# Optimization experiments

Measured on AMD Instinct MI355X. Metric: run time of the kernel, lower is better.

Reference implementation:

```python
import jax, jax.numpy as jnp
import numpy as np
from jax import lax

B, C, H, W = 32, 64, 56, 56
G = 4            # num_heads*2 with num_heads=2
SMK, K = 5, 7
C2 = C // 2
HEAD_DIM = C // G
SCALE = HEAD_DIM ** -0.5


def _bias_idx(k, h, w):
    # static replica of ContMix.generate_idx + apply_rpb index construction
    rpb_size = 2 * k - 1
    idx_h = np.arange(k)
    idx_w = np.arange(k)
    idx_k = (idx_h[:, None] * rpb_size + idx_w).reshape(-1)
    rep_h = np.ones(k, np.int64); rep_h[k // 2] = h - (k - 1)
    rep_w = np.ones(k, np.int64); rep_w[k // 2] = w - (k - 1)
    bias_hw = np.repeat(idx_h, rep_h)[:, None] * rpb_size + np.repeat(idx_w, rep_w)  # (h, w)
    bias_idx = (bias_hw[..., None] + idx_k).reshape(-1, k * k)[::-1]  # torch.flip dim 0
    return jnp.asarray(bias_idx.copy())

IDX1 = _bias_idx(SMK, H, W)
IDX2 = _bias_idx(K, H, W)


def setup_inputs() -> dict:
    key = jax.random.key(0)
    ks = jax.random.split(key, 18)
    r = lambda i, sh: jax.random.normal(ks[i], sh, jnp.float32)
    return dict(
        x=r(0, (B, C, H, W)),
        lepe_w=r(1, (C, 1, K, K)) * 0.1,
        lepe_b=r(2, (C,)) * 0.1,
        lepe_bn_s=1.0 + 0.1 * r(3, (C,)),
        lepe_bn_b=0.1 * r(4, (C,)),
        wq_w=r(5, (C2, C2)) * (C2 ** -0.5),
        wq_bn_s=1.0 + 0.1 * r(6, (C2,)),
        wq_bn_b=0.1 * r(7, (C2,)),
        wk_w=r(8, (C2, C2)) * (C2 ** -0.5),
        wk_bn_s=1.0 + 0.1 * r(9, (C2,)),
        wk_bn_b=0.1 * r(10, (C2,)),
        wp_w=r(11, (SMK * SMK + K * K, 49)) * (49 ** -0.5),
        wp_b=0.1 * r(12, (SMK * SMK + K * K,)),
        rpb1=0.02 * r(13, (G, 2 * SMK - 1, 2 * SMK - 1)),
        rpb2=0.02 * r(14, (G, 2 * K - 1, 2 * K - 1)),
        dy_w=r(15, (C, C)) * (C ** -0.5),
        dy_bn_s=1.0 + 0.1 * r(16, (C,)),
        dy_bn_b=0.1 * r(17, (C,)),
    )


def _per_ch(t):
    return t[None, :, None, None]


def _contmix(x, lepe_w, lepe_b, lepe_bn_s, lepe_bn_b, wq_w, wq_bn_s, wq_bn_b,
             wk_w, wk_bn_s, wk_bn_b, wp_w, wp_b, rpb1, rpb2, dy_w, dy_bn_s, dy_bn_b):
    # lepe: deploy-mode DilatedReparamBlock = depthwise 7x7 conv (+bias), then eval BN
    lepe = lax.conv_general_dilated(x, lepe_w, (1, 1), [(K // 2, K // 2)] * 2,
                                    feature_group_count=C)
    lepe = (lepe + _per_ch(lepe_b)) * _per_ch(lepe_bn_s) + _per_ch(lepe_bn_b)

    q, kf = jnp.split(x, 2, axis=1)                         # (B, C2, H, W) each
    q = jnp.einsum('oi,bihw->bohw', wq_w, q)                # weight_query 1x1 conv
    q = (q * _per_ch(wq_bn_s) + _per_ch(wq_bn_b)) * SCALE
    # weight_key: AdaptiveAvgPool2d(7) -> 1x1 conv -> BN (H,W divisible by 7)
    kp = kf.reshape(B, C2, 7, H // 7, 7, W // 7).mean(axis=(3, 5))
    kp = jnp.einsum('oi,bihw->bohw', wk_w, kp)
    kp = kp * _per_ch(wk_bn_s) + _per_ch(wk_bn_b)

    qg = q.reshape(B, G, C2 // G, H * W)                    # b g c n
    kg = kp.reshape(B, G, C2 // G, 49)                      # b g c l
    w = jnp.einsum('bgcn,bgcl->bgnl', qg, kg)               # (B, G, HW, 49)
    # weight_proj: 1x1 conv over the 49 pooled-context channels
    w = jnp.einsum('ml,bgnl->bgnm', wp_w, w) + wp_b         # (B, G, HW, 74)
    w = w.reshape(B, G, H, W, SMK * SMK + K * K)

    attn1 = w[..., :SMK * SMK]
    attn2 = w[..., SMK * SMK:]
    attn1 = attn1 + rpb1.reshape(G, -1)[:, IDX1].reshape(1, G, H, W, SMK * SMK)
    attn2 = attn2 + rpb2.reshape(G, -1)[:, IDX2].reshape(1, G, H, W, K * K)
    attn1 = jax.nn.softmax(attn1, axis=-1)
    attn2 = jax.nn.softmax(attn2, axis=-1)

    c = C // (2 * G)                                        # value head dim = 8
    v = x.reshape(B, 2, G, c, H, W)                         # 'b (m g c) h w'

    def dyn_mix(attn, val, k):
        # unfold + einsum: content-adaptive depthwise mixing
        p = lax.conv_general_dilated_patches(
            val.reshape(B, G * c, H, W), (k, k), (1, 1), [(k // 2, k // 2)] * 2,
            dimension_numbers=('NCHW', 'OIHW', 'NCHW'))
        p = p.reshape(B, G, c, k * k, H, W)                 # channel-major patch layout
        return jnp.einsum('bgckhw,bghwk->bgchw', p, attn)

    x1 = dyn_mix(attn1, v[:, 0], SMK)
    x2 = dyn_mix(attn2, v[:, 1], K)
    out = jnp.concatenate([x1, x2], axis=1).reshape(B, C, H, W)
    out = jnp.einsum('oi,bihw->bohw', dy_w, out)            # dyconv_proj 1x1 + BN
    out = out * _per_ch(dy_bn_s) + _per_ch(dy_bn_b)
    return out + lepe


def reference(x, lepe_w, lepe_b, lepe_bn_s, lepe_bn_b, wq_w, wq_bn_s, wq_bn_b,
              wk_w, wk_bn_s, wk_bn_b, wp_w, wp_b, rpb1, rpb2, dy_w, dy_bn_s, dy_bn_b):
    return _contmix(x, lepe_w, lepe_b, lepe_bn_s, lepe_bn_b, wq_w, wq_bn_s, wq_bn_b,
                    wk_w, wk_bn_s, wk_bn_b, wp_w, wp_b, rpb1, rpb2, dy_w, dy_bn_s, dy_bn_b)
```

## Files before the change

kernel.cpp:

```cpp
#include <hip/hip_runtime.h>

#define BB 32
#define CC 64
#define HH 56
#define WW 56
#define HW 3136
#define TW 64
#define TR 12

__global__ __launch_bounds__(256) void prep_k(const float* __restrict__ x,
                                              const float* __restrict__ wk,
                                              const float* __restrict__ wks,
                                              const float* __restrict__ wkb,
                                              const float* __restrict__ wp_w,
                                              float* __restrict__ WK) {
    __shared__ float p_s[32 * 49];
    __shared__ float kg_s[8 * 49];
    const int b = blockIdx.x >> 2;
    const int g = blockIdx.x & 3;
    const int tid = threadIdx.x;
    for (int idx = tid; idx < 1568; idx += 256) {
        const int i = idx / 49, l = idx % 49;
        const int py = l / 7, px = l % 7;
        const float4* xp4 = reinterpret_cast<const float4*>(
            x + ((long)(b * CC + 32 + i)) * HW + py * 8 * WW + px * 8);
        float4 sA = make_float4(0.f, 0.f, 0.f, 0.f);
        float4 sB = make_float4(0.f, 0.f, 0.f, 0.f);
        #pragma unroll
        for (int y = 0; y < 8; ++y) {
            const float4 a = xp4[y * 14];
            const float4 c = xp4[y * 14 + 1];
            sA.x += a.x; sA.y += a.y; sA.z += a.z; sA.w += a.w;
            sB.x += c.x; sB.y += c.y; sB.z += c.z; sB.w += c.w;
        }
        p_s[idx] = (sA.x + sA.y + sA.z + sA.w + sB.x + sB.y + sB.z + sB.w) * (1.f / 64.f);
    }
    __syncthreads();
    for (int idx = tid; idx < 392; idx += 256) {
        const int o8 = idx / 49, l = idx % 49;
        const int o = g * 8 + o8;
        float acc = 0.f;
        #pragma unroll
        for (int i = 0; i < 32; ++i) acc = fmaf(wk[o * 32 + i], p_s[i * 49 + l], acc);
        kg_s[idx] = acc * wks[o] + wkb[o];
    }
    __syncthreads();
    for (int idx = tid; idx < 640; idx += 256) {
        const int c = idx / 80, slot = idx % 80;
        float acc = 0.f;
        int m = -1;
        if (slot < 28) { if (slot < 25) m = slot; }
        else           { if (slot < 77) m = 25 + (slot - 28); }
        if (m >= 0) {
            const float* kp = kg_s + c * 49;
            #pragma unroll
            for (int l = 0; l < 49; ++l) acc = fmaf(wp_w[m * 49 + l], kp[l], acc);
        }
        const long base = (long)blockIdx.x * 640;
        if (slot < 28) WK[base + c * 28 + slot] = acc;
        else           WK[base + 224 + c * 52 + (slot - 28)] = acc;
    }
}

__global__ __launch_bounds__(256) void attnmix_k(const float* __restrict__ x,
                                                 const float* __restrict__ WK,
                                                 const float* __restrict__ wq_w,
                                                 const float* __restrict__ wq_s,
                                                 const float* __restrict__ wq_bb,
                                                 const float* __restrict__ wp_b,
                                                 const float* __restrict__ rpb1,
                                                 const float* __restrict__ rpb2,
                                                 const float* __restrict__ lw,
                                                 const float* __restrict__ lb,
                                                 const float* __restrict__ ls,
                                                 const float* __restrict__ lbb,
                                                 float* __restrict__ mix,
                                                 float* __restrict__ out) {
    __shared__ float tile[8 * TR * TW];
    __shared__ float WK1_s[8 * 28];
    __shared__ float WK2_s[8 * 52];
    __shared__ float wqT_s[32 * 8];
    __shared__ float wpb1_s[25];
    __shared__ float wpb2_s[49];
    __shared__ float rpb1_s[81];
    __shared__ float rpb2_s[169];
    __shared__ float wqbn_s[16];
    __shared__ float lw_s[16 * 49];
    __shared__ float lbn_s[48];
    const int tid = threadIdx.x;
    const int bg = blockIdx.y;
    const int g = bg & 3, b = bg >> 2;

    {
        const float* wkp = WK + (long)bg * 640;
        for (int i = tid; i < 224; i += 256) WK1_s[i] = wkp[i];
        for (int i = tid; i < 416; i += 256) WK2_s[i] = wkp[224 + i];
    }
    {
        const int i = tid >> 3, c = tid & 7;
        wqT_s[tid] = wq_w[(g * 8 + c) * 32 + i];
    }
    if (tid < 25) wpb1_s[tid] = wp_b[tid];
    if (tid >= 32 && tid < 81) wpb2_s[tid - 32] = wp_b[25 + tid - 32];
    if (tid < 81) rpb1_s[tid] = rpb1[g * 81 + tid];
    if (tid < 169) rpb2_s[tid] = rpb2[g * 169 + tid];
    if (tid >= 192 && tid < 200) wqbn_s[tid - 192] = wq_s[g * 8 + tid - 192];
    if (tid >= 200 && tid < 208) wqbn_s[8 + tid - 200] = wq_bb[g * 8 + tid - 200];
    for (int i = tid; i < 784; i += 256) {
        const int ch = i / 49, k = i % 49;
        const int c = (ch < 8) ? (g * 8 + ch) : (32 + g * 8 + ch - 8);
        lw_s[i] = lw[c * 49 + k];
    }
    if (tid < 16) {
        const int c = (tid < 8) ? (g * 8 + tid) : (32 + g * 8 + tid - 8);
        lbn_s[tid] = lb[c]; lbn_s[16 + tid] = ls[c]; lbn_s[32 + tid] = lbb[c];
    }

    const int N0 = blockIdx.x << 8;
    const int ph0 = N0 / WW;
    const int r0 = ph0 - 3;

    {
        const float* xc = x + ((long)b * CC + g * 8) * HW;
        #pragma unroll
        for (int ch = 0; ch < 8; ++ch)
            for (int k = tid; k < TR * TW; k += 256) {
                const int row = k >> 6, lxx = k & 63;
                const int gy = r0 + row, gx = lxx - 3;
                float v = 0.f;
                if ((unsigned)gy < HH && (unsigned)gx < WW) v = xc[ch * HW + gy * WW + gx];
                tile[ch * (TR * TW) + k] = v;
            }
    }
    __syncthreads();

    const int n = N0 + tid;
    const bool valid = n < HW;
    const int nc = valid ? n : HW - 1;
    const int ph = nc / WW, pw = nc % WW;
    const int yr = HH - 1 - ph, xr = WW - 1 - pw;
    const int lrow = ph - r0;
    const int tb0 = (lrow - 3) * TW + pw;

    const float* xb = x + (long)b * CC * HW + nc;

    float q8[8];
    #pragma unroll
    for (int c = 0; c < 8; ++c) q8[c] = 0.f;
    for (int i = 0; i < 32; ++i) {
        const float xv = xb[i * HW];
        #pragma unroll
        for (int c = 0; c < 8; ++c) q8[c] = fmaf(wqT_s[i * 8 + c], xv, q8[c]);
    }
    #pragma unroll
    for (int c = 0; c < 8; ++c)
        q8[c] = (q8[c] * wqbn_s[c] + wqbn_s[8 + c]) * 0.25f;

    __builtin_amdgcn_sched_barrier(0);

    {
        float w1[25];
        #pragma unroll
        for (int m = 0; m < 25; ++m) w1[m] = wpb1_s[m];
        #pragma unroll
        for (int c = 0; c < 8; ++c) {
            const float qv = q8[c];
            #pragma unroll
            for (int m = 0; m < 25; ++m) w1[m] = fmaf(qv, WK1_s[c * 28 + m], w1[m]);
        }
        const int rh5 = yr < 2 ? yr : (yr > 53 ? yr - 51 : 2);
        const int rw5 = xr < 2 ? xr : (xr > 53 ? xr - 51 : 2);
        #pragma unroll
        for (int i = 0; i < 5; ++i)
            #pragma unroll
            for (int j = 0; j < 5; ++j)
                w1[i * 5 + j] += rpb1_s[(rh5 + i) * 9 + (rw5 + j)];
        float mx = -1e30f;
        #pragma unroll
        for (int m = 0; m < 25; ++m) mx = fmaxf(mx, w1[m]);
        float sm = 0.f;
        #pragma unroll
        for (int m = 0; m < 25; ++m) { w1[m] = __expf(w1[m] - mx); sm += w1[m]; }
        const float r = 1.f / sm;
        #pragma unroll
        for (int m = 0; m < 25; ++m) w1[m] *= r;

        float* m0 = mix + ((long)b * CC + g * 8) * HW + nc;
        float* o0 = out + ((long)b * CC + g * 8) * HW + nc;
        #pragma unroll
        for (int ch = 0; ch < 8; ++ch) {
            const float* t = tile + ch * (TR * TW) + tb0;
            const float* lwc = lw_s + ch * 49;
            float a = 0.f, la = 0.f;
            #pragma unroll
            for (int i = 0; i < 7; ++i)
                #pragma unroll
                for (int j = 0; j < 7; ++j) {
                    const float v = t[i * TW + j];
                    la = fmaf(lwc[i * 7 + j], v, la);
                    if (i >= 1 && i <= 5 && j >= 1 && j <= 5)
                        a = fmaf(w1[(i - 1) * 5 + (j - 1)], v, a);
                }
            if (valid) {
                m0[ch * HW] = a;
                o0[ch * HW] = (la + lbn_s[ch]) * lbn_s[16 + ch] + lbn_s[32 + ch];
            }
        }
    }

    __syncthreads();
    {
        const float* xc = x + ((long)b * CC + 32 + g * 8) * HW;
        #pragma unroll
        for (int ch = 0; ch < 8; ++ch)
            for (int k = tid; k < TR * TW; k += 256) {
                const int row = k >> 6, lxx = k & 63;
                const int gy = r0 + row, gx = lxx - 3;
                float v = 0.f;
                if ((unsigned)gy < HH && (unsigned)gx < WW) v = xc[ch * HW + gy * WW + gx];
                tile[ch * (TR * TW) + k] = v;
            }
    }
    __syncthreads();

    {
        float w2[49];
        #pragma unroll
        for (int m = 0; m < 49; ++m) w2[m] = wpb2_s[m];
        #pragma unroll
        for (int c = 0; c < 8; ++c) {
            const float qv = q8[c];
            #pragma unroll
            for (int m = 0; m < 49; ++m) w2[m] = fmaf(qv, WK2_s[c * 52 + m], w2[m]);
        }
        const int rh7 = yr < 3 ? yr : (yr > 52 ? yr - 49 : 3);
        const int rw7 = xr < 3 ? xr : (xr > 52 ? xr - 49 : 3);
        #pragma unroll
        for (int i = 0; i < 7; ++i)
            #pragma unroll
            for (int j = 0; j < 7; ++j)
                w2[i * 7 + j] += rpb2_s[(rh7 + i) * 13 + (rw7 + j)];
        float mx = -1e30f;
        #pragma unroll
        for (int m = 0; m < 49; ++m) mx = fmaxf(mx, w2[m]);
        float sm = 0.f;
        #pragma unroll
        for (int m = 0; m < 49; ++m) { w2[m] = __expf(w2[m] - mx); sm += w2[m]; }
        const float r = 1.f / sm;
        #pragma unroll
        for (int m = 0; m < 49; ++m) w2[m] *= r;

        float* m1 = mix + ((long)b * CC + 32 + g * 8) * HW + nc;
        float* o1 = out + ((long)b * CC + 32 + g * 8) * HW + nc;
        #pragma unroll
        for (int ch = 0; ch < 8; ++ch) {
            const float* t = tile + ch * (TR * TW) + tb0;
            const float* lwc = lw_s + (8 + ch) * 49;
            float a = 0.f, la = 0.f;
            #pragma unroll
            for (int i = 0; i < 7; ++i)
                #pragma unroll
                for (int j = 0; j < 7; ++j) {
                    const float v = t[i * TW + j];
                    la = fmaf(lwc[i * 7 + j], v, la);
                    a = fmaf(w2[i * 7 + j], v, a);
                }
            if (valid) {
                m1[ch * HW] = a;
                o1[ch * HW] = (la + lbn_s[8 + ch]) * lbn_s[16 + 8 + ch] + lbn_s[32 + 8 + ch];
            }
        }
    }
}

__global__ __launch_bounds__(256) void final_k(const float* __restrict__ mix,
                                               const float* __restrict__ dy_w,
                                               const float* __restrict__ s,
                                               const float* __restrict__ bb,
                                               float* __restrict__ out) {
    __shared__ float w_s[64 * 64];
    const int tid = threadIdx.x;
    const int b = blockIdx.y;
    for (int i = tid; i < 4096; i += 256) w_s[(i & 63) * 64 + (i >> 6)] = dy_w[i];
    __syncthreads();
    const int oo = (tid >> 5) * 8;
    const int p4 = blockIdx.x * 32 + (tid & 31);
    if (p4 >= 784) return;
    const float* mp = mix + (long)b * CC * HW + p4 * 4;
    float4 acc[8];
    #pragma unroll
    for (int o = 0; o < 8; ++o) acc[o] = make_float4(0.f, 0.f, 0.f, 0.f);
    for (int i = 0; i < 64; ++i) {
        const float4 mv = *reinterpret_cast<const float4*>(mp + (long)i * HW);
        const float* wr = w_s + i * 64 + oo;
        #pragma unroll
        for (int o = 0; o < 8; ++o) {
            const float wv = wr[o];
            acc[o].x = fmaf(wv, mv.x, acc[o].x);
            acc[o].y = fmaf(wv, mv.y, acc[o].y);
            acc[o].z = fmaf(wv, mv.z, acc[o].z);
            acc[o].w = fmaf(wv, mv.w, acc[o].w);
        }
    }
    float* op = out + (long)b * CC * HW + p4 * 4;
    #pragma unroll
    for (int o = 0; o < 8; ++o) {
        const float sc = s[oo + o], bc = bb[oo + o];
        float4* dst = reinterpret_cast<float4*>(op + (long)(oo + o) * HW);
        float4 prev = *dst;
        prev.x = fmaf(acc[o].x, sc, bc) + prev.x;
        prev.y = fmaf(acc[o].y, sc, bc) + prev.y;
        prev.z = fmaf(acc[o].z, sc, bc) + prev.z;
        prev.w = fmaf(acc[o].w, sc, bc) + prev.w;
        *dst = prev;
    }
}

extern "C" void kernel_launch(void* const* d_in, const int* in_sizes, int n_in,
                              void* d_out, int out_size, void* d_ws, size_t ws_size,
                              hipStream_t stream) {
    const float* x       = (const float*)d_in[0];
    const float* lepe_w  = (const float*)d_in[1];
    const float* lepe_b  = (const float*)d_in[2];
    const float* lepe_s  = (const float*)d_in[3];
    const float* lepe_bb = (const float*)d_in[4];
    const float* wq_w    = (const float*)d_in[5];
    const float* wq_s    = (const float*)d_in[6];
    const float* wq_bb   = (const float*)d_in[7];
    const float* wk_w    = (const float*)d_in[8];
    const float* wk_s    = (const float*)d_in[9];
    const float* wk_bb   = (const float*)d_in[10];
    const float* wp_w    = (const float*)d_in[11];
    const float* wp_b    = (const float*)d_in[12];
    const float* rpb1    = (const float*)d_in[13];
    const float* rpb2    = (const float*)d_in[14];
    const float* dy_w    = (const float*)d_in[15];
    const float* dy_s    = (const float*)d_in[16];
    const float* dy_bb   = (const float*)d_in[17];
    float* out = (float*)d_out;

    float* ws     = (float*)d_ws;
    float* WK_ws  = ws;
    float* mix_ws = WK_ws + 128 * 640;

    const int nTiles = (HW + 255) / 256;

    prep_k<<<dim3(BB * 4), 256, 0, stream>>>(x, wk_w, wk_s, wk_bb, wp_w, WK_ws);
    attnmix_k<<<dim3(nTiles, BB * 4), 256, 0, stream>>>(x, WK_ws, wq_w, wq_s, wq_bb,
                                                        wp_b, rpb1, rpb2,
                                                        lepe_w, lepe_b, lepe_s, lepe_bb,
                                                        mix_ws, out);
    final_k<<<dim3(25, BB), 256, 0, stream>>>(mix_ws, dy_w, dy_s, dy_bb, out);
}
```

Before: 245.2 us.

## Precompute q in prep kernel and split attnmix into per-branch blocks

Moves the 1x1 query projection out of attnmix into extra blocks of the prep kernel, which write q to a workspace buffer. attnmix now launches twice as many blocks, each handling either the 5x5 or the 7x7 branch. This removes the second tile reload and the mid-kernel barrier, and lowers per-block register and LDS pressure. The final and q kernels also batch eight channel loads at once to expose more memory parallelism. The cost is an extra q write and read through global memory.

```diff
diff --git a/kernel.cpp b/kernel.cpp
--- a/kernel.cpp
+++ b/kernel.cpp
@@ -8,17 +8,74 @@
 #define TW 64
 #define TR 12
 
-__global__ __launch_bounds__(256) void prep_k(const float* __restrict__ x,
-                                              const float* __restrict__ wk,
-                                              const float* __restrict__ wks,
-                                              const float* __restrict__ wkb,
-                                              const float* __restrict__ wp_w,
-                                              float* __restrict__ WK) {
+__global__ __launch_bounds__(256) void prep_q_k(const float* __restrict__ x,
+                                                const float* __restrict__ wk,
+                                                const float* __restrict__ wks,
+                                                const float* __restrict__ wkb,
+                                                const float* __restrict__ wp_w,
+                                                const float* __restrict__ wq_w,
+                                                const float* __restrict__ wq_s,
+                                                const float* __restrict__ wq_bb,
+                                                float* __restrict__ WK,
+                                                float* __restrict__ qws) {
     __shared__ float p_s[32 * 49];
     __shared__ float kg_s[8 * 49];
-    const int b = blockIdx.x >> 2;
-    const int g = blockIdx.x & 3;
+    __shared__ float wqT_s[32 * 32];
+    __shared__ float qbn_s[64];
     const int tid = threadIdx.x;
+    const int bx = blockIdx.x;
+
+    if (bx < 800) {
+        for (int idx = tid; idx < 1024; idx += 256) {
+            const int o = idx & 31, i = idx >> 5;
+            wqT_s[i * 32 + o] = wq_w[o * 32 + i];
+        }
+        if (tid < 32) { qbn_s[tid] = wq_s[tid]; qbn_s[32 + tid] = wq_bb[tid]; }
+        __syncthreads();
+        const int b = bx / 25, t = bx % 25;
+        const int p4 = t * 32 + (tid & 31);
+        if (p4 >= 784) return;
+        const int oo = (tid >> 5) * 4;
+        const float* xp = x + (long)b * CC * HW + p4 * 4;
+        float4 acc[4];
+        #pragma unroll
+        for (int o = 0; o < 4; ++o) acc[o] = make_float4(0.f, 0.f, 0.f, 0.f);
+        for (int ii = 0; ii < 32; ii += 8) {
+            float4 mv[8];
+            #pragma unroll
+            for (int u = 0; u < 8; ++u)
+                mv[u] = *reinterpret_cast<const float4*>(xp + (long)(ii + u) * HW);
+            #pragma unroll
+            for (int u = 0; u < 8; ++u) {
+                const float* wr = wqT_s + (ii + u) * 32 + oo;
+                #pragma unroll
+                for (int o = 0; o < 4; ++o) {
+                    const float wv = wr[o];
+                    acc[o].x = fmaf(wv, mv[u].x, acc[o].x);
+                    acc[o].y = fmaf(wv, mv[u].y, acc[o].y);
+                    acc[o].z = fmaf(wv, mv[u].z, acc[o].z);
+                    acc[o].w = fmaf(wv, mv[u].w, acc[o].w);
+                }
+            }
+        }
+        float* qp = qws + (long)b * 32 * HW + p4 * 4;
+        #pragma unroll
+        for (int o = 0; o < 4; ++o) {
+            const float sc = qbn_s[oo + o] * 0.25f;
+            const float bc = qbn_s[32 + oo + o] * 0.25f;
+            float4 r;
+            r.x = fmaf(acc[o].x, sc, bc);
+            r.y = fmaf(acc[o].y, sc, bc);
+            r.z = fmaf(acc[o].z, sc, bc);
+            r.w = fmaf(acc[o].w, sc, bc);
+            *reinterpret_cast<float4*>(qp + (long)(oo + o) * HW) = r;
+        }
+        return;
+    }
+
+    const int id = bx - 800;
+    const int b = id >> 2;
+    const int g = id & 3;
     for (int idx = tid; idx < 1568; idx += 256) {
         const int i = idx / 49, l = idx % 49;
         const int py = l / 7, px = l % 7;
@@ -56,7 +113,7 @@
             #pragma unroll
             for (int l = 0; l < 49; ++l) acc = fmaf(wp_w[m * 49 + l], kp[l], acc);
         }
-        const long base = (long)blockIdx.x * 640;
+        const long base = (long)id * 640;
         if (slot < 28) WK[base + c * 28 + slot] = acc;
         else           WK[base + 224 + c * 52 + (slot - 28)] = acc;
     }
@@ -64,9 +121,7 @@
 
 __global__ __launch_bounds__(256) void attnmix_k(const float* __restrict__ x,
                                                  const float* __restrict__ WK,
-                                                 const float* __restrict__ wq_w,
-                                                 const float* __restrict__ wq_s,
-                                                 const float* __restrict__ wq_bb,
+                                                 const float* __restrict__ qws,
                                                  const float* __restrict__ wp_b,
                                                  const float* __restrict__ rpb1,
                                                  const float* __restrict__ rpb2,
@@ -77,51 +132,56 @@
                                                  float* __restrict__ mix,
                                                  float* __restrict__ out) {
     __shared__ float tile[8 * TR * TW];
-    __shared__ float WK1_s[8 * 28];
-    __shared__ float WK2_s[8 * 52];
-    __shared__ float wqT_s[32 * 8];
-    __shared__ float wpb1_s[25];
-    __shared__ float wpb2_s[49];
-    __shared__ float rpb1_s[81];
-    __shared__ float rpb2_s[169];
-    __shared__ float wqbn_s[16];
-    __shared__ float lw_s[16 * 49];
-    __shared__ float lbn_s[48];
+    __shared__ __align__(16) float WK_s[8 * 52];
+    __shared__ float wp_s[49];
+    __shared__ float rpb_s[169];
+    __shared__ float lw_s[8 * 49];
+    __shared__ float lbn_s[24];
     const int tid = threadIdx.x;
-    const int bg = blockIdx.y;
+    const int yb = blockIdx.y;
+    const int half = yb & 1, bg = yb >> 1;
     const int g = bg & 3, b = bg >> 2;
+    const int ch0 = (half ? 32 : 0) + g * 8;
 
     {
-        const float* wkp = WK + (long)bg * 640;
-        for (int i = tid; i < 224; i += 256) WK1_s[i] = wkp[i];
-        for (int i = tid; i < 416; i += 256) WK2_s[i] = wkp[224 + i];
-    }
-    {
-        const int i = tid >> 3, c = tid & 7;
-        wqT_s[tid] = wq_w[(g * 8 + c) * 32 + i];
-    }
-    if (tid < 25) wpb1_s[tid] = wp_b[tid];
-    if (tid >= 32 && tid < 81) wpb2_s[tid - 32] = wp_b[25 + tid - 32];
-    if (tid < 81) rpb1_s[tid] = rpb1[g * 81 + tid];
-    if (tid < 169) rpb2_s[tid] = rpb2[g * 169 + tid];
-    if (tid >= 192 && tid < 200) wqbn_s[tid - 192] = wq_s[g * 8 + tid - 192];
-    if (tid >= 200 && tid < 208) wqbn_s[8 + tid - 200] = wq_bb[g * 8 + tid - 200];
-    for (int i = tid; i < 784; i += 256) {
-        const int ch = i / 49, k = i % 49;
-        const int c = (ch < 8) ? (g * 8 + ch) : (32 + g * 8 + ch - 8);
-        lw_s[i] = lw[c * 49 + k];
-    }
-    if (tid < 16) {
-        const int c = (tid < 8) ? (g * 8 + tid) : (32 + g * 8 + tid - 8);
-        lbn_s[tid] = lb[c]; lbn_s[16 + tid] = ls[c]; lbn_s[32 + tid] = lbb[c];
+        const float* wkp = WK + (long)bg * 640 + (half ? 224 : 0);
+        const int nwk = half ? 416 : 224;
+        for (int i = tid; i < nwk; i += 256) WK_s[i] = wkp[i];
+        const int nw = half ? 49 : 25;
+        if (tid < nw) wp_s[tid] = wp_b[(half ? 25 : 0) + tid];
+        const int nr = half ? 169 : 81;
+        const float* rp = half ? (rpb2 + g * 169) : (rpb1 + g * 81);
+        if (tid < nr) rpb_s[tid] = rp[tid];
+        for (int i = tid; i < 392; i += 256) {
+            const int ch = i / 49, k = i % 49;
+            lw_s[i] = lw[(ch0 + ch) * 49 + k];
+        }
+        if (tid < 8) {
+            lbn_s[tid] = lb[ch0 + tid];
+            lbn_s[8 + tid] = ls[ch0 + tid];
+            lbn_s[16 + tid] = lbb[ch0 + tid];
+        }
     }
 
     const int N0 = blockIdx.x << 8;
     const int ph0 = N0 / WW;
     const int r0 = ph0 - 3;
 
+    const int n = N0 + tid;
+    const bool valid = n < HW;
+    const int nc = valid ? n : HW - 1;
+    const int ph = nc / WW, pw = nc % WW;
+    const int yr = HH - 1 - ph, xr = WW - 1 - pw;
+    const int lrow = ph - r0;
+    const int tb0 = (lrow - 3) * TW + pw;
+
+    const float* qp = qws + ((long)b * 32 + g * 8) * HW + nc;
+    float q8[8];
+    #pragma unroll
+    for (int c = 0; c < 8; ++c) q8[c] = qp[c * HW];
+
     {
-        const float* xc = x + ((long)b * CC + g * 8) * HW;
+        const float* xc = x + ((long)b * CC + ch0) * HW;
         #pragma unroll
         for (int ch = 0; ch < 8; ++ch)
             for (int k = tid; k < TR * TW; k += 256) {
@@ -134,39 +194,26 @@
     }
     __syncthreads();
 
-    const int n = N0 + tid;
-    const bool valid = n < HW;
-    const int nc = valid ? n : HW - 1;
-    const int ph = nc / WW, pw = nc % WW;
-    const int yr = HH - 1 - ph, xr = WW - 1 - pw;
-    const int lrow = ph - r0;
-    const int tb0 = (lrow - 3) * TW + pw;
-
-    const float* xb = x + (long)b * CC * HW + nc;
-
-    float q8[8];
-    #pragma unroll
-    for (int c = 0; c < 8; ++c) q8[c] = 0.f;
-    for (int i = 0; i < 32; ++i) {
-        const float xv = xb[i * HW];
-        #pragma unroll
-        for (int c = 0; c < 8; ++c) q8[c] = fmaf(wqT_s[i * 8 + c], xv, q8[c]);
-    }
-    #pragma unroll
-    for (int c = 0; c < 8; ++c)
-        q8[c] = (q8[c] * wqbn_s[c] + wqbn_s[8 + c]) * 0.25f;
-
-    __builtin_amdgcn_sched_barrier(0);
-
-    {
-        float w1[25];
-        #pragma unroll
-        for (int m = 0; m < 25; ++m) w1[m] = wpb1_s[m];
+    float* mp = mix + ((long)b * CC + ch0) * HW + nc;
+    float* op = out + ((long)b * CC + ch0) * HW + nc;
+
+    if (half == 0) {
+        float w1[28];
+        #pragma unroll
+        for (int m = 0; m < 25; ++m) w1[m] = wp_s[m];
+        w1[25] = w1[26] = w1[27] = 0.f;
         #pragma unroll
         for (int c = 0; c < 8; ++c) {
             const float qv = q8[c];
-            #pragma unroll
-            for (int m = 0; m < 25; ++m) w1[m] = fmaf(qv, WK1_s[c * 28 + m], w1[m]);
+            const float4* kr = reinterpret_cast<const float4*>(WK_s + c * 28);
+            #pragma unroll
+            for (int qd = 0; qd < 7; ++qd) {
+                const float4 kv = kr[qd];
+                w1[qd * 4 + 0] = fmaf(qv, kv.x, w1[qd * 4 + 0]);
+                w1[qd * 4 + 1] = fmaf(qv, kv.y, w1[qd * 4 + 1]);
+                w1[qd * 4 + 2] = fmaf(qv, kv.z, w1[qd * 4 + 2]);
+                w1[qd * 4 + 3] = fmaf(qv, kv.w, w1[qd * 4 + 3]);
+            }
         }
         const int rh5 = yr < 2 ? yr : (yr > 53 ? yr - 51 : 2);
         const int rw5 = xr < 2 ? xr : (xr > 53 ? xr - 51 : 2);
@@ -174,7 +221,7 @@
         for (int i = 0; i < 5; ++i)
             #pragma unroll
             for (int j = 0; j < 5; ++j)
-                w1[i * 5 + j] += rpb1_s[(rh5 + i) * 9 + (rw5 + j)];
+                w1[i * 5 + j] += rpb_s[(rh5 + i) * 9 + (rw5 + j)];
         float mx = -1e30f;
         #pragma unroll
         for (int m = 0; m < 25; ++m) mx = fmaxf(mx, w1[m]);
@@ -185,89 +232,83 @@
         #pragma unroll
         for (int m = 0; m < 25; ++m) w1[m] *= r;
 
-        float* m0 = mix + ((long)b * CC + g * 8) * HW + nc;
-        float* o0 = out + ((long)b * CC + g * 8) * HW + nc;
         #pragma unroll
         for (int ch = 0; ch < 8; ++ch) {
             const float* t = tile + ch * (TR * TW) + tb0;
             const float* lwc = lw_s + ch * 49;
             float a = 0.f, la = 0.f;
             #pragma unroll
-            for (int i = 0; i < 7; ++i)
+            for (int i = 0; i < 7; ++i) {
+                float v[7];
+                #pragma unroll
+                for (int j = 0; j < 7; ++j) v[j] = t[i * TW + j];
+                #pragma unroll
+                for (int j = 0; j < 7; ++j) la = fmaf(lwc[i * 7 + j], v[j], la);
+                if (i >= 1 && i <= 5) {
+                    #pragma unroll
+                    for (int j = 1; j <= 5; ++j)
+                        a = fmaf(w1[(i - 1) * 5 + (j - 1)], v[j], a);
+                }
+            }
+            if (valid) {
+                mp[ch * HW] = a;
+                op[ch * HW] = (la + lbn_s[ch]) * lbn_s[8 + ch] + lbn_s[16 + ch];
+            }
+        }
+    } else {
+        float w2[52];
+        #pragma unroll
+        for (int m = 0; m < 49; ++m) w2[m] = wp_s[m];
+        w2[49] = w2[50] = w2[51] = 0.f;
+        #pragma unroll
+        for (int c = 0; c < 8; ++c) {
+            const float qv = q8[c];
+            const float4* kr = reinterpret_cast<const float4*>(WK_s + c * 52);
+            #pragma unroll
+            for (int qd = 0; qd < 13; ++qd) {
+                const float4 kv = kr[qd];
+                w2[qd * 4 + 0] = fmaf(qv, kv.x, w2[qd * 4 + 0]);
+                w2[qd * 4 + 1] = fmaf(qv, kv.y, w2[qd * 4 + 1]);
+                w2[qd * 4 + 2] = fmaf(qv, kv.z, w2[qd * 4 + 2]);
+                w2[qd * 4 + 3] = fmaf(qv, kv.w, w2[qd * 4 + 3]);
+            }
+        }
+        const int rh7 = yr < 3 ? yr : (yr > 52 ? yr - 49 : 3);
+        const int rw7 = xr < 3 ? xr : (xr > 52 ? xr - 49 : 3);
+        #pragma unroll
+        for (int i = 0; i < 7; ++i)
+            #pragma unroll
+            for (int j = 0; j < 7; ++j)
+                w2[i * 7 + j] += rpb_s[(rh7 + i) * 13 + (rw7 + j)];
+        float mx = -1e30f;
+        #pragma unroll
+        for (int m = 0; m < 49; ++m) mx = fmaxf(mx, w2[m]);
+        float sm = 0.f;
+        #pragma unroll
+        for (int m = 0; m < 49; ++m) { w2[m] = __expf(w2[m] - mx); sm += w2[m]; }
+        const float r = 1.f / sm;
+        #pragma unroll
+        for (int m = 0; m < 49; ++m) w2[m] *= r;
+
+        #pragma unroll
+        for (int ch = 0; ch < 8; ++ch) {
+            const float* t = tile + ch * (TR * TW) + tb0;
+            const float* lwc = lw_s + ch * 49;
+            float a = 0.f, la = 0.f;
+            #pragma unroll
+            for (int i = 0; i < 7; ++i) {
+                float v[7];
+                #pragma unroll
+                for (int j = 0; j < 7; ++j) v[j] = t[i * TW + j];
                 #pragma unroll
                 for (int j = 0; j < 7; ++j) {
-                    const float v = t[i * TW + j];
-                    la = fmaf(lwc[i * 7 + j], v, la);
-                    if (i >= 1 && i <= 5 && j >= 1 && j <= 5)
-                        a = fmaf(w1[(i - 1) * 5 + (j - 1)], v, a);
+                    la = fmaf(lwc[i * 7 + j], v[j], la);
+                    a  = fmaf(w2[i * 7 + j], v[j], a);
                 }
+            }
             if (valid) {
-                m0[ch * HW] = a;
-                o0[ch * HW] = (la + lbn_s[ch]) * lbn_s[16 + ch] + lbn_s[32 + ch];
-            }
-        }
-    }
-
-    __syncthreads();
-    {
-        const float* xc = x + ((long)b * CC + 32 + g * 8) * HW;
-        #pragma unroll
-        for (int ch = 0; ch < 8; ++ch)
-            for (int k = tid; k < TR * TW; k += 256) {
-                const int row = k >> 6, lxx = k & 63;
-                const int gy = r0 + row, gx = lxx - 3;
-                float v = 0.f;
-                if ((unsigned)gy < HH && (unsigned)gx < WW) v = xc[ch * HW + gy * WW + gx];
-                tile[ch * (TR * TW) + k] = v;
-            }
-    }
-    __syncthreads();
-
-    {
-        float w2[49];
-        #pragma unroll
-        for (int m = 0; m < 49; ++m) w2[m] = wpb2_s[m];
-        #pragma unroll
-        for (int c = 0; c < 8; ++c) {
-            const float qv = q8[c];
-            #pragma unroll
-            for (int m = 0; m < 49; ++m) w2[m] = fmaf(qv, WK2_s[c * 52 + m], w2[m]);
-        }
-        const int rh7 = yr < 3 ? yr : (yr > 52 ? yr - 49 : 3);
-        const int rw7 = xr < 3 ? xr : (xr > 52 ? xr - 49 : 3);
-        #pragma unroll
-        for (int i = 0; i < 7; ++i)
-            #pragma unroll
-            for (int j = 0; j < 7; ++j)
-                w2[i * 7 + j] += rpb2_s[(rh7 + i) * 13 + (rw7 + j)];
-        float mx = -1e30f;
-        #pragma unroll
-        for (int m = 0; m < 49; ++m) mx = fmaxf(mx, w2[m]);
-        float sm = 0.f;
-        #pragma unroll
-        for (int m = 0; m < 49; ++m) { w2[m] = __expf(w2[m] - mx); sm += w2[m]; }
-        const float r = 1.f / sm;
-        #pragma unroll
-        for (int m = 0; m < 49; ++m) w2[m] *= r;
-
-        float* m1 = mix + ((long)b * CC + 32 + g * 8) * HW + nc;
-        float* o1 = out + ((long)b * CC + 32 + g * 8) * HW + nc;
-        #pragma unroll
-        for (int ch = 0; ch < 8; ++ch) {
-            const float* t = tile + ch * (TR * TW) + tb0;
-            const float* lwc = lw_s + (8 + ch) * 49;
-            float a = 0.f, la = 0.f;
-            #pragma unroll
-            for (int i = 0; i < 7; ++i)
-                #pragma unroll
-                for (int j = 0; j < 7; ++j) {
-                    const float v = t[i * TW + j];
-                    la = fmaf(lwc[i * 7 + j], v, la);
-                    a = fmaf(w2[i * 7 + j], v, a);
-                }
-            if (valid) {
-                m1[ch * HW] = a;
-                o1[ch * HW] = (la + lbn_s[8 + ch]) * lbn_s[16 + 8 + ch] + lbn_s[32 + 8 + ch];
+                mp[ch * HW] = a;
+                op[ch * HW] = (la + lbn_s[ch]) * lbn_s[8 + ch] + lbn_s[16 + ch];
             }
         }
     }
@@ -290,16 +331,22 @@
     float4 acc[8];
     #pragma unroll
     for (int o = 0; o < 8; ++o) acc[o] = make_float4(0.f, 0.f, 0.f, 0.f);
-    for (int i = 0; i < 64; ++i) {
-        const float4 mv = *reinterpret_cast<const float4*>(mp + (long)i * HW);
-        const float* wr = w_s + i * 64 + oo;
-        #pragma unroll
-        for (int o = 0; o < 8; ++o) {
-            const float wv = wr[o];
-            acc[o].x = fmaf(wv, mv.x, acc[o].x);
-            acc[o].y = fmaf(wv, mv.y, acc[o].y);
-            acc[o].z = fmaf(wv, mv.z, acc[o].z);
-            acc[o].w = fmaf(wv, mv.w, acc[o].w);
+    for (int ii = 0; ii < 64; ii += 8) {
+        float4 mv[8];
+        #pragma unroll
+        for (int u = 0; u < 8; ++u)
+            mv[u] = *reinterpret_cast<const float4*>(mp + (long)(ii + u) * HW);
+        #pragma unroll
+        for (int u = 0; u < 8; ++u) {
+            const float* wr = w_s + (ii + u) * 64 + oo;
+            #pragma unroll
+            for (int o = 0; o < 8; ++o) {
+                const float wv = wr[o];
+                acc[o].x = fmaf(wv, mv[u].x, acc[o].x);
+                acc[o].y = fmaf(wv, mv[u].y, acc[o].y);
+                acc[o].z = fmaf(wv, mv[u].z, acc[o].z);
+                acc[o].w = fmaf(wv, mv[u].w, acc[o].w);
+            }
         }
     }
     float* op = out + (long)b * CC * HW + p4 * 4;
@@ -341,14 +388,16 @@
 
     float* ws     = (float*)d_ws;
     float* WK_ws  = ws;
-    float* mix_ws = WK_ws + 128 * 640;
+    float* q_ws   = WK_ws + 128 * 640;
+    float* mix_ws = q_ws + 32 * 32 * HW;
 
     const int nTiles = (HW + 255) / 256;
 
-    prep_k<<<dim3(BB * 4), 256, 0, stream>>>(x, wk_w, wk_s, wk_bb, wp_w, WK_ws);
-    attnmix_k<<<dim3(nTiles, BB * 4), 256, 0, stream>>>(x, WK_ws, wq_w, wq_s, wq_bb,
-                                                        wp_b, rpb1, rpb2,
-                                                        lepe_w, lepe_b, lepe_s, lepe_bb,
-                                                        mix_ws, out);
+    prep_q_k<<<dim3(800 + BB * 4), 256, 0, stream>>>(x, wk_w, wk_s, wk_bb, wp_w,
+                                                     wq_w, wq_s, wq_bb, WK_ws, q_ws);
+    attnmix_k<<<dim3(nTiles, BB * 4 * 2), 256, 0, stream>>>(x, WK_ws, q_ws,
+                                                            wp_b, rpb1, rpb2,
+                                                            lepe_w, lepe_b, lepe_s, lepe_bb,
+                                                            mix_ws, out);
     final_k<<<dim3(25, BB), 256, 0, stream>>>(mix_ws, dy_w, dy_s, dy_bb, out);
 }
```

Result: slower. 267.5 us (+9.1%).

## Hold attention weights in VGPRs and broadcast via readlane; batch loads in final_k

Applied to the files above, without the earlier changes.

In attnmix_k, the per-block weight tables (q projection, BN params, wp bias, WK1/WK2, lepe weights) no longer live in LDS. Each lane now holds a slice in registers, and values are broadcast with readlane. This removes many LDS reads from the inner FMA loops and shrinks shared memory, and the first barrier is deferred so the q computation can overlap the tile fill. In final_k, eight channel rows are loaded before the FMAs to raise memory-level parallelism. The costs are higher VGPR/SGPR pressure and many readlane instructions, which may serialize or lower occupancy.

```diff
diff --git a/kernel.cpp b/kernel.cpp
--- a/kernel.cpp
+++ b/kernel.cpp
@@ -7,6 +7,11 @@
 #define HW 3136
 #define TW 64
 #define TR 12
+
+__device__ __forceinline__ float RL1(float src, int lane) {
+    return __int_as_float(__builtin_amdgcn_readlane(__float_as_int(src), lane));
+}
+#define RLA(arr, idx) RL1(arr[(idx) >> 6], (idx) & 63)
 
 __global__ __launch_bounds__(256) void prep_k(const float* __restrict__ x,
                                               const float* __restrict__ wk,
@@ -77,48 +82,66 @@
                                                  float* __restrict__ mix,
                                                  float* __restrict__ out) {
     __shared__ float tile[8 * TR * TW];
-    __shared__ float WK1_s[8 * 28];
-    __shared__ float WK2_s[8 * 52];
-    __shared__ float wqT_s[32 * 8];
-    __shared__ float wpb1_s[25];
-    __shared__ float wpb2_s[49];
     __shared__ float rpb1_s[81];
     __shared__ float rpb2_s[169];
-    __shared__ float wqbn_s[16];
-    __shared__ float lw_s[16 * 49];
-    __shared__ float lbn_s[48];
     const int tid = threadIdx.x;
+    const int lane = tid & 63;
     const int bg = blockIdx.y;
     const int g = bg & 3, b = bg >> 2;
 
-    {
-        const float* wkp = WK + (long)bg * 640;
-        for (int i = tid; i < 224; i += 256) WK1_s[i] = wkp[i];
-        for (int i = tid; i < 416; i += 256) WK2_s[i] = wkp[224 + i];
-    }
-    {
-        const int i = tid >> 3, c = tid & 7;
-        wqT_s[tid] = wq_w[(g * 8 + c) * 32 + i];
-    }
-    if (tid < 25) wpb1_s[tid] = wp_b[tid];
-    if (tid >= 32 && tid < 81) wpb2_s[tid - 32] = wp_b[25 + tid - 32];
     if (tid < 81) rpb1_s[tid] = rpb1[g * 81 + tid];
     if (tid < 169) rpb2_s[tid] = rpb2[g * 169 + tid];
-    if (tid >= 192 && tid < 200) wqbn_s[tid - 192] = wq_s[g * 8 + tid - 192];
-    if (tid >= 200 && tid < 208) wqbn_s[8 + tid - 200] = wq_bb[g * 8 + tid - 200];
-    for (int i = tid; i < 784; i += 256) {
-        const int ch = i / 49, k = i % 49;
-        const int c = (ch < 8) ? (g * 8 + ch) : (32 + g * 8 + ch - 8);
-        lw_s[i] = lw[c * 49 + k];
-    }
-    if (tid < 16) {
-        const int c = (tid < 8) ? (g * 8 + tid) : (32 + g * 8 + tid - 8);
-        lbn_s[tid] = lb[c]; lbn_s[16 + tid] = ls[c]; lbn_s[32 + tid] = lbb[c];
+
+    float wqT_r[4];
+    #pragma unroll
+    for (int r = 0; r < 4; ++r) {
+        const int idx = r * 64 + lane, i = idx >> 3, c = idx & 7;
+        wqT_r[r] = wq_w[(g * 8 + c) * 32 + i];
+    }
+    float wqbn_r;
+    {
+        const int c = lane & 7;
+        wqbn_r = (lane < 8) ? wq_s[g * 8 + c] : (lane < 16 ? wq_bb[g * 8 + c] : 0.f);
+    }
+    float wpb_r[2];
+    #pragma unroll
+    for (int r = 0; r < 2; ++r) {
+        const int idx = r * 64 + lane;
+        wpb_r[r] = (idx < 74) ? wp_b[idx] : 0.f;
+    }
+    const float* wkp = WK + (long)bg * 640;
+    float wk1_r[4];
+    #pragma unroll
+    for (int r = 0; r < 4; ++r) {
+        const int idx = r * 64 + lane;
+        wk1_r[r] = (idx < 224) ? wkp[idx] : 0.f;
+    }
+    float lw1_r[7];
+    #pragma unroll
+    for (int r = 0; r < 7; ++r) {
+        const int idx = r * 64 + lane;
+        lw1_r[r] = (idx < 392) ? lw[(g * 8) * 49 + idx] : 0.f;
+    }
+    float lbn_r;
+    {
+        const int which = lane >> 4, c16 = lane & 15;
+        const int ch = (c16 < 8) ? (g * 8 + c16) : (32 + g * 8 + (c16 - 8));
+        lbn_r = (which == 0) ? lb[ch] : (which == 1) ? ls[ch] : (which == 2) ? lbb[ch] : 0.f;
     }
 
     const int N0 = blockIdx.x << 8;
     const int ph0 = N0 / WW;
     const int r0 = ph0 - 3;
+
+    const int n = N0 + tid;
+    const bool valid = n < HW;
+    const int nc = valid ? n : HW - 1;
+    const int ph = nc / WW, pw = nc % WW;
+    const int yr = HH - 1 - ph, xr = WW - 1 - pw;
+    const int lrow = ph - r0;
+    const int tb0 = (lrow - 3) * TW + pw;
+
+    const float* xb = x + (long)b * CC * HW + nc;
 
     {
         const float* xc = x + ((long)b * CC + g * 8) * HW;
@@ -132,17 +155,6 @@
                 tile[ch * (TR * TW) + k] = v;
             }
     }
-    __syncthreads();
-
-    const int n = N0 + tid;
-    const bool valid = n < HW;
-    const int nc = valid ? n : HW - 1;
-    const int ph = nc / WW, pw = nc % WW;
-    const int yr = HH - 1 - ph, xr = WW - 1 - pw;
-    const int lrow = ph - r0;
-    const int tb0 = (lrow - 3) * TW + pw;
-
-    const float* xb = x + (long)b * CC * HW + nc;
 
     float q8[8];
     #pragma unroll
@@ -150,23 +162,23 @@
     for (int i = 0; i < 32; ++i) {
         const float xv = xb[i * HW];
         #pragma unroll
-        for (int c = 0; c < 8; ++c) q8[c] = fmaf(wqT_s[i * 8 + c], xv, q8[c]);
+        for (int c = 0; c < 8; ++c) q8[c] = fmaf(RLA(wqT_r, i * 8 + c), xv, q8[c]);
     }
     #pragma unroll
     for (int c = 0; c < 8; ++c)
-        q8[c] = (q8[c] * wqbn_s[c] + wqbn_s[8 + c]) * 0.25f;
-
-    __builtin_amdgcn_sched_barrier(0);
+        q8[c] = fmaf(q8[c], RL1(wqbn_r, c), RL1(wqbn_r, 8 + c)) * 0.25f;
+
+    __syncthreads();
 
     {
         float w1[25];
         #pragma unroll
-        for (int m = 0; m < 25; ++m) w1[m] = wpb1_s[m];
+        for (int m = 0; m < 25; ++m) w1[m] = RLA(wpb_r, m);
         #pragma unroll
         for (int c = 0; c < 8; ++c) {
             const float qv = q8[c];
             #pragma unroll
-            for (int m = 0; m < 25; ++m) w1[m] = fmaf(qv, WK1_s[c * 28 + m], w1[m]);
+            for (int m = 0; m < 25; ++m) w1[m] = fmaf(qv, RLA(wk1_r, c * 28 + m), w1[m]);
         }
         const int rh5 = yr < 2 ? yr : (yr > 53 ? yr - 51 : 2);
         const int rw5 = xr < 2 ? xr : (xr > 53 ? xr - 51 : 2);
@@ -190,22 +202,34 @@
         #pragma unroll
         for (int ch = 0; ch < 8; ++ch) {
             const float* t = tile + ch * (TR * TW) + tb0;
-            const float* lwc = lw_s + ch * 49;
             float a = 0.f, la = 0.f;
             #pragma unroll
             for (int i = 0; i < 7; ++i)
                 #pragma unroll
                 for (int j = 0; j < 7; ++j) {
                     const float v = t[i * TW + j];
-                    la = fmaf(lwc[i * 7 + j], v, la);
+                    la = fmaf(RLA(lw1_r, ch * 49 + i * 7 + j), v, la);
                     if (i >= 1 && i <= 5 && j >= 1 && j <= 5)
                         a = fmaf(w1[(i - 1) * 5 + (j - 1)], v, a);
                 }
             if (valid) {
                 m0[ch * HW] = a;
-                o0[ch * HW] = (la + lbn_s[ch]) * lbn_s[16 + ch] + lbn_s[32 + ch];
-            }
-        }
+                o0[ch * HW] = (la + RL1(lbn_r, ch)) * RL1(lbn_r, 16 + ch) + RL1(lbn_r, 32 + ch);
+            }
+        }
+    }
+
+    float wk2_r[7];
+    #pragma unroll
+    for (int r = 0; r < 7; ++r) {
+        const int idx = r * 64 + lane;
+        wk2_r[r] = (idx < 416) ? wkp[224 + idx] : 0.f;
+    }
+    float lw2_r[7];
+    #pragma unroll
+    for (int r = 0; r < 7; ++r) {
+        const int idx = r * 64 + lane;
+        lw2_r[r] = (idx < 392) ? lw[(32 + g * 8) * 49 + idx] : 0.f;
     }
 
     __syncthreads();
@@ -226,12 +250,12 @@
     {
         float w2[49];
         #pragma unroll
-        for (int m = 0; m < 49; ++m) w2[m] = wpb2_s[m];
+        for (int m = 0; m < 49; ++m) w2[m] = RLA(wpb_r, 25 + m);
         #pragma unroll
         for (int c = 0; c < 8; ++c) {
             const float qv = q8[c];
             #pragma unroll
-            for (int m = 0; m < 49; ++m) w2[m] = fmaf(qv, WK2_s[c * 52 + m], w2[m]);
+            for (int m = 0; m < 49; ++m) w2[m] = fmaf(qv, RLA(wk2_r, c * 52 + m), w2[m]);
         }
         const int rh7 = yr < 3 ? yr : (yr > 52 ? yr - 49 : 3);
         const int rw7 = xr < 3 ? xr : (xr > 52 ? xr - 49 : 3);
@@ -255,19 +279,18 @@
         #pragma unroll
         for (int ch = 0; ch < 8; ++ch) {
             const float* t = tile + ch * (TR * TW) + tb0;
-            const float* lwc = lw_s + (8 + ch) * 49;
             float a = 0.f, la = 0.f;
             #pragma unroll
             for (int i = 0; i < 7; ++i)
                 #pragma unroll
                 for (int j = 0; j < 7; ++j) {
                     const float v = t[i * TW + j];
-                    la = fmaf(lwc[i * 7 + j], v, la);
-                    a = fmaf(w2[i * 7 + j], v, a);
+                    la = fmaf(RLA(lw2_r, ch * 49 + i * 7 + j), v, la);
+                    a  = fmaf(w2[i * 7 + j], v, a);
                 }
             if (valid) {
                 m1[ch * HW] = a;
-                o1[ch * HW] = (la + lbn_s[8 + ch]) * lbn_s[16 + 8 + ch] + lbn_s[32 + 8 + ch];
+                o1[ch * HW] = (la + RL1(lbn_r, 8 + ch)) * RL1(lbn_r, 24 + ch) + RL1(lbn_r, 40 + ch);
             }
         }
     }
@@ -290,16 +313,22 @@
     float4 acc[8];
     #pragma unroll
     for (int o = 0; o < 8; ++o) acc[o] = make_float4(0.f, 0.f, 0.f, 0.f);
-    for (int i = 0; i < 64; ++i) {
-        const float4 mv = *reinterpret_cast<const float4*>(mp + (long)i * HW);
-        const float* wr = w_s + i * 64 + oo;
-        #pragma unroll
-        for (int o = 0; o < 8; ++o) {
-            const float wv = wr[o];
-            acc[o].x = fmaf(wv, mv.x, acc[o].x);
-            acc[o].y = fmaf(wv, mv.y, acc[o].y);
-            acc[o].z = fmaf(wv, mv.z, acc[o].z);
-            acc[o].w = fmaf(wv, mv.w, acc[o].w);
+    for (int ii = 0; ii < 64; ii += 8) {
+        float4 mv[8];
+        #pragma unroll
+        for (int u = 0; u < 8; ++u)
+            mv[u] = *reinterpret_cast<const float4*>(mp + (long)(ii + u) * HW);
+        #pragma unroll
+        for (int u = 0; u < 8; ++u) {
+            const float* wr = w_s + (ii + u) * 64 + oo;
+            #pragma unroll
+            for (int o = 0; o < 8; ++o) {
+                const float wv = wr[o];
+                acc[o].x = fmaf(wv, mv[u].x, acc[o].x);
+                acc[o].y = fmaf(wv, mv[u].y, acc[o].y);
+                acc[o].z = fmaf(wv, mv[u].z, acc[o].z);
+                acc[o].w = fmaf(wv, mv[u].w, acc[o].w);
+            }
         }
     }
     float* op = out + (long)b * CC * HW + p4 * 4;
```

Measured after the change: 237.2 us. 3.3% less time.
